# Optimization experiments

Hardware: AMD Instinct MI355X
Metric: run time of the kernel (lower is better)

Reference implementation:

```python
import math
import jax, jax.numpy as jnp
import numpy as np

UNITS = 256
D_IN = 256
BATCH = 65536
STRENGTH = 0.5
PERIOD = 25.0
LAMBDA_SLOW = 0.1
JITTER = 0.05
H_INERTIA = 0.9
REST_BASELINE = 1.0


def setup_inputs() -> dict:
    key = jax.random.key(0)
    k1, k2, k3, k4, k5, k6 = jax.random.split(key, 6)
    glorot = math.sqrt(2.0 / (D_IN + UNITS))
    return {
        "inputs": jax.random.normal(k1, (BATCH, D_IN), dtype=jnp.float32),
        "prev_h": jax.random.normal(k2, (BATCH, UNITS), dtype=jnp.float32),
        "prev_G": jax.random.normal(k3, (BATCH, UNITS), dtype=jnp.float32),
        "prev_phase": jax.random.normal(k4, (BATCH, 1), dtype=jnp.float32),
        "w_in": jax.random.normal(k5, (D_IN, UNITS), dtype=jnp.float32) * glorot,
        "w_rec": jax.random.normal(k6, (UNITS, UNITS), dtype=jnp.float32) * (1.0 / math.sqrt(UNITS)),
        "bias": jnp.zeros((UNITS,), dtype=jnp.float32),
    }


def reference(inputs, prev_h, prev_G, prev_phase, w_in, w_rec, bias):
    half = UNITS // 2
    # roll-like swap of the two halves of the hidden state
    raw_signal = jnp.concatenate([prev_h[:, half:], prev_h[:, :half]], axis=1)
    # slow exponential-moving-average field
    new_G = (1.0 - LAMBDA_SLOW) * prev_G + LAMBDA_SLOW * raw_signal
    mean = jnp.mean(new_G, axis=-1, keepdims=True)
    std = jnp.std(new_G, axis=-1, keepdims=True)  # population std, matches tf.math.reduce_std
    G_norm = (new_G - mean) / (std + 1e-6)
    new_phase = prev_phase + 2.0 * math.pi / PERIOD
    oscillator = jnp.sin(new_phase)
    bias_signal = jnp.mean(raw_signal, axis=-1, keepdims=True) - 0.1
    combined_signal = oscillator + JITTER * bias_signal
    field_effect = REST_BASELINE + STRENGTH * combined_signal * jnp.tanh(G_norm)
    z = (inputs @ w_in + prev_h @ w_rec + bias) * field_effect
    h = H_INERTIA * prev_h + (1.0 - H_INERTIA) * jax.nn.elu(z)
    h = jnp.clip(h, -20.0, 20.0)
    return (h, new_G, new_phase)
```

## Files before the change

kernel.cpp:

```cpp
#include <hip/hip_runtime.h>

typedef unsigned short ushort_t;
typedef short v8s __attribute__((ext_vector_type(8)));
typedef float v4f __attribute__((ext_vector_type(4)));

#define BATCH    65536
#define UNITS    256
#define M_TILE   32
#define KSTEPS   16
#define BCHUNK   10240
#define T_STRIDE 264
#define LDS_HB   0
#define LDS_GT   16896
#define LDS_SC   33792
#define LDS_TOT  35200

__device__ __forceinline__ float b2f(ushort_t u) {
    union { unsigned int i; float f; } v; v.i = ((unsigned int)u) << 16; return v.f;
}
__device__ __forceinline__ ushort_t f2b(float f) {
    union { float f; unsigned int i; } v; v.f = f;
    unsigned int r = (v.i + 0x7fffu + ((v.i >> 16) & 1u)) >> 16;
    return (ushort_t)r;
}

__global__ void pack_w(const float* __restrict__ w_in,
                       const float* __restrict__ w_rec,
                       ushort_t* __restrict__ Wp) {
    int gid = blockIdx.x * 256 + threadIdx.x;
    int k = gid >> 8, n = gid & 255;
    float v = (k < 256) ? w_in[k * 256 + n] : w_rec[(k - 256) * 256 + n];
    Wp[(size_t)(k >> 5) * BCHUNK + n * 40 + (k & 31)] = f2b(v);
}

__global__ __launch_bounds__(256, 4)
void fused_cell(const float* __restrict__ inputs,
                const float* __restrict__ prev_h,
                const float* __restrict__ prev_G,
                const float* __restrict__ prev_phase,
                const ushort_t* __restrict__ Wp,
                const float* __restrict__ bias,
                float* __restrict__ out) {
    __shared__ __align__(16) char smem[LDS_TOT];
    short* Hb     = (short*)(smem + LDS_HB);
    short* Gt     = (short*)(smem + LDS_GT);
    float* r_mean = (float*)(smem + LDS_SC);
    float* r_rstd = r_mean + 32;
    float* r_comb = r_rstd + 32;
    float* bias_f = r_comb + 32;

    const int tid  = threadIdx.x;
    const int row0 = blockIdx.x * M_TILE;

    float* outH = out;
    float* outG = out + (size_t)BATCH * UNITS;
    float* outP = out + (size_t)2 * BATCH * UNITS;

    bias_f[tid] = bias[tid];

    {
        const int lr = tid >> 3;
        const int p  = tid & 7;
        const int gr = row0 + lr;
        float s1 = 0.f, s2 = 0.f, sh = 0.f;
        #pragma unroll
        for (int i = 0; i < 8; ++i) {
            int c0 = i * 32 + p * 4;
            int pc = (c0 + 128) & 255;
            float4 hp = *(const float4*)(prev_h + (size_t)gr * UNITS + pc);
            float4 gp = *(const float4*)(prev_G + (size_t)gr * UNITS + c0);
            float4 ng;
            ng.x = 0.9f * gp.x + 0.1f * hp.x;
            ng.y = 0.9f * gp.y + 0.1f * hp.y;
            ng.z = 0.9f * gp.z + 0.1f * hp.z;
            ng.w = 0.9f * gp.w + 0.1f * hp.w;
            s1 += ng.x + ng.y + ng.z + ng.w;
            s2 += ng.x*ng.x + ng.y*ng.y + ng.z*ng.z + ng.w*ng.w;
            sh += hp.x + hp.y + hp.z + hp.w;
            *(float4*)(outG + (size_t)gr * UNITS + c0) = ng;
            ushort4 gq; gq.x = f2b(ng.x); gq.y = f2b(ng.y); gq.z = f2b(ng.z); gq.w = f2b(ng.w);
            *(ushort4*)(Gt + lr * T_STRIDE + c0) = gq;
            ushort4 hq; hq.x = f2b(hp.x); hq.y = f2b(hp.y); hq.z = f2b(hp.z); hq.w = f2b(hp.w);
            *(ushort4*)(Hb + lr * T_STRIDE + pc) = hq;
        }
        #pragma unroll
        for (int off = 4; off > 0; off >>= 1) {
            s1 += __shfl_xor(s1, off, 64);
            s2 += __shfl_xor(s2, off, 64);
            sh += __shfl_xor(sh, off, 64);
        }
        if (p == 0) {
            float mean = s1 * (1.f / 256.f);
            float var  = s2 * (1.f / 256.f) - mean * mean;
            float rstd = 1.f / (sqrtf(fmaxf(var, 0.f)) + 1e-6f);
            float np   = prev_phase[gr] + 0.2513274122871834591f;
            outP[gr] = np;
            float comb = sinf(np) + 0.05f * (sh * (1.f / 256.f) - 0.1f);
            r_mean[lr] = mean; r_rstd[lr] = rstd; r_comb[lr] = comb;
        }
    }

    __syncthreads();

    const int l   = tid & 63;
    const int w   = tid >> 6;
    const int n16 = l & 15;
    const int q   = l >> 4;
    const int rg  = w & 1;
    const int ch  = w >> 1;

    v4f acc[8];
    const v4f z4 = {0.f, 0.f, 0.f, 0.f};
    #pragma unroll
    for (int t = 0; t < 8; ++t) acc[t] = z4;

    const int arow = rg * 16 + n16;
    const float* ainp = inputs + (size_t)(row0 + arow) * UNITS + q * 8;
    const short* hbp  = Hb + arow * T_STRIDE + q * 8;
    const short* bp   = (const short*)Wp + (ch * 128 + n16) * 40 + q * 8;

    #pragma unroll 2
    for (int s = 0; s < KSTEPS; ++s) {
        v8s a;
        if (s < 8) {
            float4 f0 = *(const float4*)(ainp + s * 32);
            float4 f1 = *(const float4*)(ainp + s * 32 + 4);
            a[0] = (short)f2b(f0.x); a[1] = (short)f2b(f0.y);
            a[2] = (short)f2b(f0.z); a[3] = (short)f2b(f0.w);
            a[4] = (short)f2b(f1.x); a[5] = (short)f2b(f1.y);
            a[6] = (short)f2b(f1.z); a[7] = (short)f2b(f1.w);
        } else {
            a = *(const v8s*)(hbp + (s - 8) * 32);
        }
        const short* bs = bp + s * BCHUNK;
        #pragma unroll
        for (int t = 0; t < 8; ++t) {
            v8s b = *(const v8s*)(bs + t * 640);
            acc[t] = __builtin_amdgcn_mfma_f32_16x16x32_bf16(a, b, acc[t], 0, 0, 0);
        }
    }

    #pragma unroll
    for (int t = 0; t < 8; ++t) {
        int c = ch * 128 + t * 16 + n16;
        float bz = bias_f[c];
        #pragma unroll
        for (int r = 0; r < 4; ++r) {
            int lr = rg * 16 + q * 4 + r;
            int gr = row0 + lr;
            float gval = b2f((ushort_t)Gt[lr * T_STRIDE + c]);
            float gn = (gval - r_mean[lr]) * r_rstd[lr];
            float e2 = __expf(2.f * gn);
            float th = 1.f - 2.f / (e2 + 1.f);
            float field = 1.f + 0.5f * r_comb[lr] * th;
            float z = (acc[t][r] + bz) * field;
            float el = (z > 0.f) ? z : (__expf(z) - 1.f);
            float h = 0.9f * b2f((ushort_t)Hb[lr * T_STRIDE + c]) + 0.1f * el;
            h = fminf(fmaxf(h, -20.f), 20.f);
            outH[(size_t)gr * UNITS + c] = h;
        }
    }
}

extern "C" void kernel_launch(void* const* d_in, const int* in_sizes, int n_in,
                              void* d_out, int out_size, void* d_ws, size_t ws_size,
                              hipStream_t stream) {
    const float* inputs     = (const float*)d_in[0];
    const float* prev_h     = (const float*)d_in[1];
    const float* prev_G     = (const float*)d_in[2];
    const float* prev_phase = (const float*)d_in[3];
    const float* w_in       = (const float*)d_in[4];
    const float* w_rec      = (const float*)d_in[5];
    const float* bias       = (const float*)d_in[6];
    float* out    = (float*)d_out;
    ushort_t* Wp  = (ushort_t*)d_ws;

    pack_w<<<512, 256, 0, stream>>>(w_in, w_rec, Wp);
    fused_cell<<<BATCH / M_TILE, 256, 0, stream>>>(inputs, prev_h, prev_G,
                                                   prev_phase, Wp, bias, out);
}
```

Baseline: 329.3 us.

## Stage inputs in LDS and split MFMA work by column across waves

The inputs tile is now converted to bf16 during the prologue and staged in LDS next to prev_h, in a k-major padded layout, so the MFMA loop reads A fragments only from LDS. Each wave now owns 64 output columns across all 32 rows, reusing each B fragment for two MFMAs, which halves global weight loads per block. The weights are pre-packed into a lane-contiguous fragment layout so each B load is a fully coalesced 16-byte read. LDS use per block grows to about 70 KB, and launch bounds drop to 3 blocks per CU, which may reduce latency hiding.

```diff
diff --git a/kernel.cpp b/kernel.cpp
--- a/kernel.cpp
+++ b/kernel.cpp
@@ -7,13 +7,14 @@
 #define BATCH    65536
 #define UNITS    256
 #define M_TILE   32
-#define KSTEPS   16
-#define BCHUNK   10240
-#define T_STRIDE 264
-#define LDS_HB   0
-#define LDS_GT   16896
-#define LDS_SC   33792
-#define LDS_TOT  35200
+#define A_PAD    33
+#define GT_STRIDE 264
+#define LDS_A    0
+#define LDS_A_SZ (64 * A_PAD * 16)
+#define LDS_GT   LDS_A_SZ
+#define LDS_GT_SZ (32 * GT_STRIDE * 2)
+#define LDS_SC   (LDS_GT + LDS_GT_SZ)
+#define LDS_TOT  (LDS_SC + 1408)
 
 __device__ __forceinline__ float b2f(ushort_t u) {
     union { unsigned int i; float f; } v; v.i = ((unsigned int)u) << 16; return v.f;
@@ -30,10 +31,12 @@
     int gid = blockIdx.x * 256 + threadIdx.x;
     int k = gid >> 8, n = gid & 255;
     float v = (k < 256) ? w_in[k * 256 + n] : w_rec[(k - 256) * 256 + n];
-    Wp[(size_t)(k >> 5) * BCHUNK + n * 40 + (k & 31)] = f2b(v);
+    int s = k >> 5, t = n >> 4;
+    int lane = ((k >> 3) & 3) * 16 + (n & 15);
+    Wp[(size_t)(((s * 16 + t) * 64) + lane) * 8 + (k & 7)] = f2b(v);
 }
 
-__global__ __launch_bounds__(256, 4)
+__global__ __launch_bounds__(256, 3)
 void fused_cell(const float* __restrict__ inputs,
                 const float* __restrict__ prev_h,
                 const float* __restrict__ prev_G,
@@ -42,7 +45,7 @@
                 const float* __restrict__ bias,
                 float* __restrict__ out) {
     __shared__ __align__(16) char smem[LDS_TOT];
-    short* Hb     = (short*)(smem + LDS_HB);
+    short* Ak     = (short*)(smem + LDS_A);
     short* Gt     = (short*)(smem + LDS_GT);
     float* r_mean = (float*)(smem + LDS_SC);
     float* r_rstd = r_mean + 32;
@@ -67,8 +70,14 @@
         for (int i = 0; i < 8; ++i) {
             int c0 = i * 32 + p * 4;
             int pc = (c0 + 128) & 255;
+            float4 xi = *(const float4*)(inputs + (size_t)gr * UNITS + c0);
             float4 hp = *(const float4*)(prev_h + (size_t)gr * UNITS + pc);
             float4 gp = *(const float4*)(prev_G + (size_t)gr * UNITS + c0);
+            ushort4 xq; xq.x = f2b(xi.x); xq.y = f2b(xi.y); xq.z = f2b(xi.z); xq.w = f2b(xi.w);
+            *(ushort4*)(Ak + ((c0 >> 3) * A_PAD + lr) * 8 + (c0 & 7)) = xq;
+            ushort4 hq; hq.x = f2b(hp.x); hq.y = f2b(hp.y); hq.z = f2b(hp.z); hq.w = f2b(hp.w);
+            int kh = 256 + pc;
+            *(ushort4*)(Ak + ((kh >> 3) * A_PAD + lr) * 8 + (pc & 7)) = hq;
             float4 ng;
             ng.x = 0.9f * gp.x + 0.1f * hp.x;
             ng.y = 0.9f * gp.y + 0.1f * hp.y;
@@ -79,9 +88,7 @@
             sh += hp.x + hp.y + hp.z + hp.w;
             *(float4*)(outG + (size_t)gr * UNITS + c0) = ng;
             ushort4 gq; gq.x = f2b(ng.x); gq.y = f2b(ng.y); gq.z = f2b(ng.z); gq.w = f2b(ng.w);
-            *(ushort4*)(Gt + lr * T_STRIDE + c0) = gq;
-            ushort4 hq; hq.x = f2b(hp.x); hq.y = f2b(hp.y); hq.z = f2b(hp.z); hq.w = f2b(hp.w);
-            *(ushort4*)(Hb + lr * T_STRIDE + pc) = hq;
+            *(ushort4*)(Gt + lr * GT_STRIDE + c0) = gq;
         }
         #pragma unroll
         for (int off = 4; off > 0; off >>= 1) {
@@ -106,58 +113,52 @@
     const int w   = tid >> 6;
     const int n16 = l & 15;
     const int q   = l >> 4;
-    const int rg  = w & 1;
-    const int ch  = w >> 1;
 
-    v4f acc[8];
+    v4f acc[2][4];
     const v4f z4 = {0.f, 0.f, 0.f, 0.f};
     #pragma unroll
-    for (int t = 0; t < 8; ++t) acc[t] = z4;
+    for (int mi = 0; mi < 2; ++mi)
+        #pragma unroll
+        for (int t = 0; t < 4; ++t) acc[mi][t] = z4;
 
-    const int arow = rg * 16 + n16;
-    const float* ainp = inputs + (size_t)(row0 + arow) * UNITS + q * 8;
-    const short* hbp  = Hb + arow * T_STRIDE + q * 8;
-    const short* bp   = (const short*)Wp + (ch * 128 + n16) * 40 + q * 8;
+    const short* ap = Ak + (q * A_PAD + n16) * 8;
+    const short* bw = (const short*)Wp + ((size_t)(w * 4) * 64 + l) * 8;
 
     #pragma unroll 2
-    for (int s = 0; s < KSTEPS; ++s) {
-        v8s a;
-        if (s < 8) {
-            float4 f0 = *(const float4*)(ainp + s * 32);
-            float4 f1 = *(const float4*)(ainp + s * 32 + 4);
-            a[0] = (short)f2b(f0.x); a[1] = (short)f2b(f0.y);
-            a[2] = (short)f2b(f0.z); a[3] = (short)f2b(f0.w);
-            a[4] = (short)f2b(f1.x); a[5] = (short)f2b(f1.y);
-            a[6] = (short)f2b(f1.z); a[7] = (short)f2b(f1.w);
-        } else {
-            a = *(const v8s*)(hbp + (s - 8) * 32);
-        }
-        const short* bs = bp + s * BCHUNK;
+    for (int s = 0; s < 16; ++s) {
+        v8s a0 = *(const v8s*)(ap + s * (4 * A_PAD * 8));
+        v8s a1 = *(const v8s*)(ap + s * (4 * A_PAD * 8) + 128);
         #pragma unroll
-        for (int t = 0; t < 8; ++t) {
-            v8s b = *(const v8s*)(bs + t * 640);
-            acc[t] = __builtin_amdgcn_mfma_f32_16x16x32_bf16(a, b, acc[t], 0, 0, 0);
+        for (int t = 0; t < 4; ++t) {
+            v8s b = *(const v8s*)(bw + (s * 16 + t) * 512);
+            acc[0][t] = __builtin_amdgcn_mfma_f32_16x16x32_bf16(a0, b, acc[0][t], 0, 0, 0);
+            acc[1][t] = __builtin_amdgcn_mfma_f32_16x16x32_bf16(a1, b, acc[1][t], 0, 0, 0);
         }
     }
 
     #pragma unroll
-    for (int t = 0; t < 8; ++t) {
-        int c = ch * 128 + t * 16 + n16;
-        float bz = bias_f[c];
+    for (int mi = 0; mi < 2; ++mi) {
         #pragma unroll
-        for (int r = 0; r < 4; ++r) {
-            int lr = rg * 16 + q * 4 + r;
-            int gr = row0 + lr;
-            float gval = b2f((ushort_t)Gt[lr * T_STRIDE + c]);
-            float gn = (gval - r_mean[lr]) * r_rstd[lr];
-            float e2 = __expf(2.f * gn);
-            float th = 1.f - 2.f / (e2 + 1.f);
-            float field = 1.f + 0.5f * r_comb[lr] * th;
-            float z = (acc[t][r] + bz) * field;
-            float el = (z > 0.f) ? z : (__expf(z) - 1.f);
-            float h = 0.9f * b2f((ushort_t)Hb[lr * T_STRIDE + c]) + 0.1f * el;
-            h = fminf(fmaxf(h, -20.f), 20.f);
-            outH[(size_t)gr * UNITS + c] = h;
+        for (int t = 0; t < 4; ++t) {
+            int c = (w * 4 + t) * 16 + n16;
+            float bz = bias_f[c];
+            #pragma unroll
+            for (int r = 0; r < 4; ++r) {
+                int lr = mi * 16 + q * 4 + r;
+                int gr = row0 + lr;
+                float gval = b2f((ushort_t)Gt[lr * GT_STRIDE + c]);
+                float gn = (gval - r_mean[lr]) * r_rstd[lr];
+                float e2 = __expf(2.f * gn);
+                float th = 1.f - 2.f / (e2 + 1.f);
+                float field = 1.f + 0.5f * r_comb[lr] * th;
+                float z = (acc[mi][t][r] + bz) * field;
+                float el = (z > 0.f) ? z : (__expf(z) - 1.f);
+                int kh = 256 + c;
+                float hprev = b2f((ushort_t)Ak[((kh >> 3) * A_PAD + lr) * 8 + (c & 7)]);
+                float h = 0.9f * hprev + 0.1f * el;
+                h = fminf(fmaxf(h, -20.f), 20.f);
+                outH[(size_t)gr * UNITS + c] = h;
+            }
         }
     }
 }
```

Result: faster. 318.1 us (-3.4%).

## Give each wave its own 16-row tile and drop the block barrier

Applied to the files above, without the earlier changes.

Each wave now owns 16 rows and computes all 256 output columns (16 accumulators), so the block-wide __syncthreads is removed. Row statistics and the G tile are kept per wave in LDS. Weights are repacked into a fragment-major layout so each lane does one coalesced 16-byte load per MFMA. prev_h is no longer staged as bf16 in LDS; it is re-read from global memory in fp32 for both the MFMA operand and the final update, which also uses full-precision h in the blend. In exchange the accumulator register footprint doubles (launch bounds lowered to 2) and global traffic for prev_h rises.

```diff
diff --git a/kernel.cpp b/kernel.cpp
--- a/kernel.cpp
+++ b/kernel.cpp
@@ -6,14 +6,7 @@
 
 #define BATCH    65536
 #define UNITS    256
-#define M_TILE   32
-#define KSTEPS   16
-#define BCHUNK   10240
-#define T_STRIDE 264
-#define LDS_HB   0
-#define LDS_GT   16896
-#define LDS_SC   33792
-#define LDS_TOT  35200
+#define GT_STRIDE 264
 
 __device__ __forceinline__ float b2f(ushort_t u) {
     union { unsigned int i; float f; } v; v.i = ((unsigned int)u) << 16; return v.f;
@@ -30,10 +23,12 @@
     int gid = blockIdx.x * 256 + threadIdx.x;
     int k = gid >> 8, n = gid & 255;
     float v = (k < 256) ? w_in[k * 256 + n] : w_rec[(k - 256) * 256 + n];
-    Wp[(size_t)(k >> 5) * BCHUNK + n * 40 + (k & 31)] = f2b(v);
+    int s = k >> 5, t = n >> 4;
+    int lane = ((k >> 3) & 3) * 16 + (n & 15);
+    Wp[(size_t)(((s * 16 + t) * 64) + lane) * 8 + (k & 7)] = f2b(v);
 }
 
-__global__ __launch_bounds__(256, 4)
+__global__ __launch_bounds__(256, 2)
 void fused_cell(const float* __restrict__ inputs,
                 const float* __restrict__ prev_h,
                 const float* __restrict__ prev_G,
@@ -41,34 +36,35 @@
                 const ushort_t* __restrict__ Wp,
                 const float* __restrict__ bias,
                 float* __restrict__ out) {
-    __shared__ __align__(16) char smem[LDS_TOT];
-    short* Hb     = (short*)(smem + LDS_HB);
-    short* Gt     = (short*)(smem + LDS_GT);
-    float* r_mean = (float*)(smem + LDS_SC);
-    float* r_rstd = r_mean + 32;
-    float* r_comb = r_rstd + 32;
-    float* bias_f = r_comb + 32;
+    __shared__ __align__(16) short Gt[64 * GT_STRIDE];
+    __shared__ float r_mean[64], r_rstd[64], r_comb[64];
 
-    const int tid  = threadIdx.x;
-    const int row0 = blockIdx.x * M_TILE;
+    const int tid = threadIdx.x;
+    const int w   = tid >> 6;
+    const int l   = tid & 63;
+    const int wr0 = blockIdx.x * 64 + w * 16;
 
     float* outH = out;
     float* outG = out + (size_t)BATCH * UNITS;
     float* outP = out + (size_t)2 * BATCH * UNITS;
 
-    bias_f[tid] = bias[tid];
+    short* GtW = Gt + (w * 16) * GT_STRIDE;
 
+    const int prow = l >> 2;
+    const int p    = l & 3;
+    const int gr1  = wr0 + prow;
+
+    float s1 = 0.f, s2 = 0.f, sh = 0.f;
     {
-        const int lr = tid >> 3;
-        const int p  = tid & 7;
-        const int gr = row0 + lr;
-        float s1 = 0.f, s2 = 0.f, sh = 0.f;
+        const float* hpR = prev_h + (size_t)gr1 * UNITS;
+        const float* gpR = prev_G + (size_t)gr1 * UNITS;
+        float*       ogR = outG  + (size_t)gr1 * UNITS;
         #pragma unroll
-        for (int i = 0; i < 8; ++i) {
-            int c0 = i * 32 + p * 4;
+        for (int i = 0; i < 16; ++i) {
+            int c0 = i * 16 + p * 4;
             int pc = (c0 + 128) & 255;
-            float4 hp = *(const float4*)(prev_h + (size_t)gr * UNITS + pc);
-            float4 gp = *(const float4*)(prev_G + (size_t)gr * UNITS + c0);
+            float4 hp = *(const float4*)(hpR + pc);
+            float4 gp = *(const float4*)(gpR + c0);
             float4 ng;
             ng.x = 0.9f * gp.x + 0.1f * hp.x;
             ng.y = 0.9f * gp.y + 0.1f * hp.y;
@@ -77,85 +73,96 @@
             s1 += ng.x + ng.y + ng.z + ng.w;
             s2 += ng.x*ng.x + ng.y*ng.y + ng.z*ng.z + ng.w*ng.w;
             sh += hp.x + hp.y + hp.z + hp.w;
-            *(float4*)(outG + (size_t)gr * UNITS + c0) = ng;
-            ushort4 gq; gq.x = f2b(ng.x); gq.y = f2b(ng.y); gq.z = f2b(ng.z); gq.w = f2b(ng.w);
-            *(ushort4*)(Gt + lr * T_STRIDE + c0) = gq;
-            ushort4 hq; hq.x = f2b(hp.x); hq.y = f2b(hp.y); hq.z = f2b(hp.z); hq.w = f2b(hp.w);
-            *(ushort4*)(Hb + lr * T_STRIDE + pc) = hq;
-        }
-        #pragma unroll
-        for (int off = 4; off > 0; off >>= 1) {
-            s1 += __shfl_xor(s1, off, 64);
-            s2 += __shfl_xor(s2, off, 64);
-            sh += __shfl_xor(sh, off, 64);
-        }
-        if (p == 0) {
-            float mean = s1 * (1.f / 256.f);
-            float var  = s2 * (1.f / 256.f) - mean * mean;
-            float rstd = 1.f / (sqrtf(fmaxf(var, 0.f)) + 1e-6f);
-            float np   = prev_phase[gr] + 0.2513274122871834591f;
-            outP[gr] = np;
-            float comb = sinf(np) + 0.05f * (sh * (1.f / 256.f) - 0.1f);
-            r_mean[lr] = mean; r_rstd[lr] = rstd; r_comb[lr] = comb;
+            *(float4*)(ogR + c0) = ng;
+            ushort4 gq; gq.x = f2b(ng.x); gq.y = f2b(ng.y);
+            gq.z = f2b(ng.z); gq.w = f2b(ng.w);
+            *(ushort4*)(GtW + prow * GT_STRIDE + c0) = gq;
         }
     }
+    s1 += __shfl_xor(s1, 1, 64); s1 += __shfl_xor(s1, 2, 64);
+    s2 += __shfl_xor(s2, 1, 64); s2 += __shfl_xor(s2, 2, 64);
+    sh += __shfl_xor(sh, 1, 64); sh += __shfl_xor(sh, 2, 64);
+    if (p == 0) {
+        float mean = s1 * (1.f / 256.f);
+        float var  = s2 * (1.f / 256.f) - mean * mean;
+        float rstd = 1.f / (sqrtf(fmaxf(var, 0.f)) + 1e-6f);
+        float np   = prev_phase[gr1] + 0.2513274122871834591f;
+        float comb = sinf(np) + 0.05f * (sh * (1.f / 256.f) - 0.1f);
+        outP[gr1] = np;
+        int lrow = w * 16 + prow;
+        r_mean[lrow] = mean; r_rstd[lrow] = rstd; r_comb[lrow] = comb;
+    }
 
-    __syncthreads();
-
-    const int l   = tid & 63;
-    const int w   = tid >> 6;
     const int n16 = l & 15;
     const int q   = l >> 4;
-    const int rg  = w & 1;
-    const int ch  = w >> 1;
+    const float* ainp = inputs + (size_t)(wr0 + n16) * UNITS + q * 8;
+    const float* ahp  = prev_h + (size_t)(wr0 + n16) * UNITS + q * 8;
+    const short* bw   = (const short*)Wp + l * 8;
 
-    v4f acc[8];
+    v4f acc[16];
     const v4f z4 = {0.f, 0.f, 0.f, 0.f};
     #pragma unroll
-    for (int t = 0; t < 8; ++t) acc[t] = z4;
-
-    const int arow = rg * 16 + n16;
-    const float* ainp = inputs + (size_t)(row0 + arow) * UNITS + q * 8;
-    const short* hbp  = Hb + arow * T_STRIDE + q * 8;
-    const short* bp   = (const short*)Wp + (ch * 128 + n16) * 40 + q * 8;
+    for (int t = 0; t < 16; ++t) acc[t] = z4;
 
     #pragma unroll 2
-    for (int s = 0; s < KSTEPS; ++s) {
+    for (int s = 0; s < 8; ++s) {
+        float4 f0 = *(const float4*)(ainp + s * 32);
+        float4 f1 = *(const float4*)(ainp + s * 32 + 4);
         v8s a;
-        if (s < 8) {
-            float4 f0 = *(const float4*)(ainp + s * 32);
-            float4 f1 = *(const float4*)(ainp + s * 32 + 4);
-            a[0] = (short)f2b(f0.x); a[1] = (short)f2b(f0.y);
-            a[2] = (short)f2b(f0.z); a[3] = (short)f2b(f0.w);
-            a[4] = (short)f2b(f1.x); a[5] = (short)f2b(f1.y);
-            a[6] = (short)f2b(f1.z); a[7] = (short)f2b(f1.w);
-        } else {
-            a = *(const v8s*)(hbp + (s - 8) * 32);
+        a[0] = (short)f2b(f0.x); a[1] = (short)f2b(f0.y);
+        a[2] = (short)f2b(f0.z); a[3] = (short)f2b(f0.w);
+        a[4] = (short)f2b(f1.x); a[5] = (short)f2b(f1.y);
+        a[6] = (short)f2b(f1.z); a[7] = (short)f2b(f1.w);
+        const short* bs = bw + s * 8192;
+        #pragma unroll
+        for (int t = 0; t < 16; ++t) {
+            v8s b = *(const v8s*)(bs + t * 512);
+            acc[t] = __builtin_amdgcn_mfma_f32_16x16x32_bf16(a, b, acc[t], 0, 0, 0);
         }
-        const short* bs = bp + s * BCHUNK;
+    }
+    #pragma unroll 2
+    for (int s = 8; s < 16; ++s) {
+        float4 f0 = *(const float4*)(ahp + (s - 8) * 32);
+        float4 f1 = *(const float4*)(ahp + (s - 8) * 32 + 4);
+        v8s a;
+        a[0] = (short)f2b(f0.x); a[1] = (short)f2b(f0.y);
+        a[2] = (short)f2b(f0.z); a[3] = (short)f2b(f0.w);
+        a[4] = (short)f2b(f1.x); a[5] = (short)f2b(f1.y);
+        a[6] = (short)f2b(f1.z); a[7] = (short)f2b(f1.w);
+        const short* bs = bw + s * 8192;
         #pragma unroll
-        for (int t = 0; t < 8; ++t) {
-            v8s b = *(const v8s*)(bs + t * 640);
+        for (int t = 0; t < 16; ++t) {
+            v8s b = *(const v8s*)(bs + t * 512);
             acc[t] = __builtin_amdgcn_mfma_f32_16x16x32_bf16(a, b, acc[t], 0, 0, 0);
         }
     }
 
+    float m_[4], rs_[4], cb_[4];
     #pragma unroll
-    for (int t = 0; t < 8; ++t) {
-        int c = ch * 128 + t * 16 + n16;
-        float bz = bias_f[c];
+    for (int r = 0; r < 4; ++r) {
+        int lrr = w * 16 + q * 4 + r;
+        m_[r]  = r_mean[lrr];
+        rs_[r] = r_rstd[lrr];
+        cb_[r] = r_comb[lrr];
+    }
+
+    #pragma unroll
+    for (int t = 0; t < 16; ++t) {
+        int c = t * 16 + n16;
+        float bz = bias[c];
         #pragma unroll
         for (int r = 0; r < 4; ++r) {
-            int lr = rg * 16 + q * 4 + r;
-            int gr = row0 + lr;
-            float gval = b2f((ushort_t)Gt[lr * T_STRIDE + c]);
-            float gn = (gval - r_mean[lr]) * r_rstd[lr];
+            int lr = q * 4 + r;
+            int gr = wr0 + lr;
+            float gval = b2f((ushort_t)GtW[lr * GT_STRIDE + c]);
+            float gn = (gval - m_[r]) * rs_[r];
             float e2 = __expf(2.f * gn);
             float th = 1.f - 2.f / (e2 + 1.f);
-            float field = 1.f + 0.5f * r_comb[lr] * th;
+            float field = 1.f + 0.5f * cb_[r] * th;
             float z = (acc[t][r] + bz) * field;
             float el = (z > 0.f) ? z : (__expf(z) - 1.f);
-            float h = 0.9f * b2f((ushort_t)Hb[lr * T_STRIDE + c]) + 0.1f * el;
+            float hprev = prev_h[(size_t)gr * UNITS + c];
+            float h = 0.9f * hprev + 0.1f * el;
             h = fminf(fmaxf(h, -20.f), 20.f);
             outH[(size_t)gr * UNITS + c] = h;
         }
@@ -176,6 +183,6 @@
     ushort_t* Wp  = (ushort_t*)d_ws;
 
     pack_w<<<512, 256, 0, stream>>>(w_in, w_rec, Wp);
-    fused_cell<<<BATCH / M_TILE, 256, 0, stream>>>(inputs, prev_h, prev_G,
-                                                   prev_phase, Wp, bias, out);
+    fused_cell<<<BATCH / 64, 256, 0, stream>>>(inputs, prev_h, prev_G,
+                                               prev_phase, Wp, bias, out);
 }
```

Result: slower. 376.5 us (+14.3%).
